# Optimization experiments

Hardware: AMD Instinct MI355X
Metric: run time of the kernel (lower is better)

The kernel has to match this reference:

```python
import jax, jax.numpy as jnp
import numpy as np
from jax import lax

WIRES = 4
EPS = 1e-5


def _conv2d(x, w, b):
    # x: [B,C,H,W], w: [O,I,3,3], SAME padding, stride 1
    y = lax.conv_general_dilated(x, w, (1, 1), 'SAME',
                                 dimension_numbers=('NCHW', 'OIHW', 'NCHW'))
    return y + b[None, :, None, None]


def _maxpool2(x):
    return lax.reduce_window(x, -jnp.inf, lax.max, (1, 1, 2, 2), (1, 1, 2, 2), 'VALID')


def _cnot_perm(c, t, n=WIRES):
    # wire 0 = most significant bit; CNOT is a self-inverse basis permutation
    idx = np.arange(2 ** n)
    cbit = (idx >> (n - 1 - c)) & 1
    flipped = idx ^ (1 << (n - 1 - t))
    return np.where(cbit == 1, flipped, idx)


_CNOT_PERMS = [_cnot_perm(c, c + 1) for c in range(WIRES - 1)]
_Z_SIGNS = np.stack([1.0 - 2.0 * ((np.arange(2 ** WIRES) >> (WIRES - 1 - i)) & 1)
                     for i in range(WIRES)], axis=1).astype(np.float32)  # [16, 4]


def _quantum_circuit(q_params, feats):
    # Batched state-vector sim of: RY(feats[i]) wire i; RX(params[i]) wire i;
    # CNOT chain; <Z_i>.  feats: [B,4], q_params: [4]
    hf = 0.5 * feats
    hp = 0.5 * q_params
    cy, sy = jnp.cos(hf), jnp.sin(hf)            # [B,4]
    cx, sx = jnp.cos(hp), jnp.sin(hp)            # [4]
    # per-wire state after RX @ RY |0>: amplitudes of |0>, |1>
    a0 = (cx * cy - 1j * sx * sy).astype(jnp.complex64)  # [B,4]
    a1 = (cx * sy - 1j * sx * cy).astype(jnp.complex64)  # [B,4]
    single = jnp.stack([a0, a1], axis=-1)        # [B,4,2]
    # product state -> full 16-dim state via successive outer products
    psi = single[:, 0]                           # [B,2]
    for i in range(1, WIRES):
        psi = (psi[:, :, None] * single[:, i][:, None, :]).reshape(psi.shape[0], -1)
    # CNOT chain = fixed basis permutations
    for perm in _CNOT_PERMS:
        psi = psi[:, perm]                       # [B,16]
    probs = psi.real ** 2 + psi.imag ** 2        # [B,16]
    return probs @ jnp.asarray(_Z_SIGNS)         # [B,4]


def setup_inputs() -> dict:
    key = jax.random.key(0)
    ks = jax.random.split(key, 8)
    B, C, H, W = 512, 1, 128, 128
    return {
        'x': jax.random.normal(ks[0], (B, C, H, W), jnp.float32),
        'conv1_w': jax.random.normal(ks[1], (8, C, 3, 3), jnp.float32) * 0.1,
        'conv1_b': jnp.zeros((8,), jnp.float32),
        'conv2_w': jax.random.normal(ks[2], (16, 8, 3, 3), jnp.float32) * 0.1,
        'conv2_b': jnp.zeros((16,), jnp.float32),
        'q_params': jax.random.normal(ks[3], (WIRES,), jnp.float32),
        'bn_gamma': jnp.ones((4,), jnp.float32),
        'bn_beta': jnp.zeros((4,), jnp.float32),
        'head_w': jax.random.normal(ks[4], (4, WIRES), jnp.float32) * 0.5,
        'head_b': jnp.zeros((4,), jnp.float32),
    }


def reference(x, conv1_w, conv1_b, conv2_w, conv2_b, q_params,
              bn_gamma, bn_beta, head_w, head_b):
    h = jax.nn.relu(_conv2d(x, conv1_w, conv1_b))
    h = _maxpool2(h)
    h = jax.nn.relu(_conv2d(h, conv2_w, conv2_b))
    h = _maxpool2(h)
    feats = h.mean(axis=(2, 3))                  # AdaptiveAvgPool2d(1) -> [B,16]
    q_out = _quantum_circuit(q_params, feats[:, :WIRES])  # [B,4]
    # BatchNorm1d (training mode, biased variance)
    mu = q_out.mean(axis=0)
    var = q_out.var(axis=0)
    normed = bn_gamma * (q_out - mu) / jnp.sqrt(var + EPS) + bn_beta
    return normed @ head_w.T + head_b
```

## Files before the change

### kernel.cpp

```cpp
#include <hip/hip_runtime.h>

#define EPS 1e-5f

typedef float f2 __attribute__((ext_vector_type(2)));
typedef float f4 __attribute__((ext_vector_type(4)));

__device__ __forceinline__ float uload(const float* __restrict__ p) {
  return __int_as_float(__builtin_amdgcn_readfirstlane(__float_as_int(*p)));
}

__global__ __launch_bounds__(256, 4) void k12_fused(
    const float* __restrict__ x, const float* __restrict__ w1,
    const float* __restrict__ b1, const float* __restrict__ w2,
    const float* __restrict__ b2, float* __restrict__ partials) {
  __shared__ float p1[8][18][66];
  __shared__ float wred[4][4];

  const int q   = blockIdx.x & 3;
  const int b   = blockIdx.x >> 2;
  const int tid = threadIdx.x;
  const float* xb = x + (size_t)b * (128 * 128);

  if (tid < 144) {
    int ic = tid / 18, gl = tid - ic * 18;
    p1[ic][gl][0]  = 0.f;
    p1[ic][gl][65] = 0.f;
  }

  float wv1[8][9], bb1[8];
#pragma unroll
  for (int oc = 0; oc < 8; ++oc) {
#pragma unroll
    for (int k = 0; k < 9; ++k) wv1[oc][k] = uload(w1 + oc * 9 + k);
    bb1[oc] = uload(b1 + oc);
  }

#pragma unroll 1
  for (int pos = tid; pos < 18 * 64; pos += 256) {
    const int gl = pos >> 6, px = pos & 63;
    const int G = 16 * q - 1 + gl;
    const bool validG = (G >= 0) && (G < 64);
    const int xr0 = 2 * G - 1;
    float xin[4][4];
#pragma unroll
    for (int r = 0; r < 4; ++r) {
      const int row = xr0 + r;
      const bool rok = validG && (row >= 0) && (row < 128);
      const float* rp = xb + row * 128;
#pragma unroll
      for (int c = 0; c < 4; ++c) {
        const int col = 2 * px - 1 + c;
        const bool ok = rok && (col >= 0) && (col < 128);
        xin[r][c] = ok ? rp[col] : 0.f;
      }
    }
#pragma unroll
    for (int oc = 0; oc < 8; ++oc) {
      float best = 0.f;
#pragma unroll
      for (int dy = 0; dy < 2; ++dy)
#pragma unroll
        for (int dx = 0; dx < 2; ++dx) {
          float a = bb1[oc];
#pragma unroll
          for (int ky = 0; ky < 3; ++ky)
#pragma unroll
            for (int kx = 0; kx < 3; ++kx)
              a = fmaf(xin[dy + ky][dx + kx], wv1[oc][ky * 3 + kx], a);
          best = fmaxf(best, a);
        }
      p1[oc][gl][px + 1] = validG ? best : 0.f;
    }
  }
  __syncthreads();

  const int px2  = tid & 31;
  const int py2l = tid >> 5;

  float acc[4][2][2];
#pragma unroll
  for (int oc = 0; oc < 4; ++oc) {
    float bias = uload(b2 + oc);
    acc[oc][0][0] = bias; acc[oc][0][1] = bias;
    acc[oc][1][0] = bias; acc[oc][1][1] = bias;
  }

#pragma unroll 1
  for (int ic = 0; ic < 8; ++ic) {
    float xin[4][4];
#pragma unroll
    for (int r = 0; r < 4; ++r) {
      const f2* rp = (const f2*)&p1[ic][2 * py2l + r][2 * px2];
      f2 v0 = rp[0], v1 = rp[1];
      xin[r][0] = v0.x; xin[r][1] = v0.y; xin[r][2] = v1.x; xin[r][3] = v1.y;
    }
#pragma unroll
    for (int oc = 0; oc < 4; ++oc) {
      float wv[9];
#pragma unroll
      for (int k = 0; k < 9; ++k) wv[k] = uload(w2 + (oc * 8 + ic) * 9 + k);
#pragma unroll
      for (int dy = 0; dy < 2; ++dy)
#pragma unroll
        for (int dx = 0; dx < 2; ++dx) {
#pragma unroll
          for (int ky = 0; ky < 3; ++ky)
#pragma unroll
            for (int kx = 0; kx < 3; ++kx)
              acc[oc][dy][dx] =
                  fmaf(xin[dy + ky][dx + kx], wv[ky * 3 + kx], acc[oc][dy][dx]);
        }
    }
  }

  const int lane = tid & 63, w = tid >> 6;
#pragma unroll
  for (int oc = 0; oc < 4; ++oc) {
    float p = fmaxf(fmaxf(fmaxf(acc[oc][0][0], acc[oc][0][1]),
                          fmaxf(acc[oc][1][0], acc[oc][1][1])), 0.f);
#pragma unroll
    for (int off = 32; off > 0; off >>= 1) p += __shfl_down(p, off);
    if (lane == 0) wred[w][oc] = p;
  }
  __syncthreads();
  if (tid < 4) {
    float s = wred[0][tid] + wred[1][tid] + wred[2][tid] + wred[3][tid];
    partials[((size_t)b * 4 + q) * 4 + tid] = s;
  }
}

__global__ __launch_bounds__(512) void k3_tail(
    const float* __restrict__ partials, const float* __restrict__ qp,
    const float* __restrict__ gamma, const float* __restrict__ beta,
    const float* __restrict__ hw, const float* __restrict__ hb,
    float* __restrict__ out) {
  __shared__ float wsum[8][8];
  __shared__ float stats[8];
  const int tid = threadIdx.x;

  const f4* pp = (const f4*)(partials + tid * 16);
  f4 s0 = pp[0], s1 = pp[1], s2 = pp[2], s3 = pp[3];
  float f[4];
  f[0] = (s0.x + s1.x + s2.x + s3.x) * (1.f / 1024.f);
  f[1] = (s0.y + s1.y + s2.y + s3.y) * (1.f / 1024.f);
  f[2] = (s0.z + s1.z + s2.z + s3.z) * (1.f / 1024.f);
  f[3] = (s0.w + s1.w + s2.w + s3.w) * (1.f / 1024.f);

  float a0r[4], a0i[4], a1r[4], a1i[4];
#pragma unroll
  for (int i = 0; i < 4; ++i) {
    float cy, sy, cx, sx;
    __sincosf(0.5f * f[i], &sy, &cy);
    __sincosf(0.5f * uload(qp + i), &sx, &cx);
    a0r[i] = cx * cy; a0i[i] = -sx * sy;
    a1r[i] = cx * sy; a1i[i] = -sx * cy;
  }

  float pr[16], pi[16];
#pragma unroll
  for (int j = 0; j < 16; ++j) {
    float rr = 1.f, ii = 0.f;
#pragma unroll
    for (int w = 0; w < 4; ++w) {
      int bit = (j >> (3 - w)) & 1;
      float ar = bit ? a1r[w] : a0r[w];
      float ai = bit ? a1i[w] : a0i[w];
      float t = rr * ar - ii * ai;
      ii = rr * ai + ii * ar;
      rr = t;
    }
    pr[j] = rr; pi[j] = ii;
  }

  constexpr int comp[16] = {0, 1, 3, 2, 6, 7, 5, 4, 12, 13, 15, 14, 10, 11, 9, 8};
  float qv[4] = {0.f, 0.f, 0.f, 0.f};
#pragma unroll
  for (int j = 0; j < 16; ++j) {
    int s = comp[j];
    float p = pr[s] * pr[s] + pi[s] * pi[s];
#pragma unroll
    for (int i = 0; i < 4; ++i)
      qv[i] += ((j >> (3 - i)) & 1) ? -p : p;
  }

  float v[8];
#pragma unroll
  for (int i = 0; i < 4; ++i) { v[i] = qv[i]; v[4 + i] = qv[i] * qv[i]; }
#pragma unroll
  for (int k = 0; k < 8; ++k)
#pragma unroll
    for (int off = 32; off > 0; off >>= 1) v[k] += __shfl_down(v[k], off);
  const int lane = tid & 63, w = tid >> 6;
  if (lane == 0) {
#pragma unroll
    for (int k = 0; k < 8; ++k) wsum[w][k] = v[k];
  }
  __syncthreads();
  if (tid < 8) {
    float s = 0.f;
#pragma unroll
    for (int ww = 0; ww < 8; ++ww) s += wsum[ww][tid];
    stats[tid] = s * (1.f / 512.f);
  }
  __syncthreads();

  float nm[4];
#pragma unroll
  for (int i = 0; i < 4; ++i) {
    float mu  = stats[i];
    float var = stats[4 + i] - mu * mu;
    nm[i] = uload(gamma + i) * (qv[i] - mu) * rsqrtf(var + EPS) + uload(beta + i);
  }
#pragma unroll
  for (int k = 0; k < 4; ++k) {
    float o = uload(hb + k);
#pragma unroll
    for (int i = 0; i < 4; ++i) o = fmaf(nm[i], uload(hw + k * 4 + i), o);
    out[tid * 4 + k] = o;
  }
}

extern "C" void kernel_launch(void* const* d_in, const int* in_sizes, int n_in,
                              void* d_out, int out_size, void* d_ws, size_t ws_size,
                              hipStream_t stream) {
  const float* x  = (const float*)d_in[0];
  const float* w1 = (const float*)d_in[1];
  const float* b1 = (const float*)d_in[2];
  const float* w2 = (const float*)d_in[3];
  const float* b2 = (const float*)d_in[4];
  const float* qp = (const float*)d_in[5];
  const float* gm = (const float*)d_in[6];
  const float* bt = (const float*)d_in[7];
  const float* hw = (const float*)d_in[8];
  const float* hb = (const float*)d_in[9];
  float* out = (float*)d_out;

  float* partials = (float*)d_ws;

  k12_fused<<<512 * 4, 256, 0, stream>>>(x, w1, b1, w2, b2, partials);
  k3_tail<<<1, 512, 0, stream>>>(partials, qp, gm, bt, hw, hb, out);
}
```

Before: 124.8 us.

## Stage input tile in LDS and split conv1/conv2 into two channel groups

Each block first copies its input row band (38x130 with zero halo) into shared memory, so conv1 reads LDS instead of gathering overlapping global loads. Conv1 and conv2 then run in two passes of four channels each, which halves the p1 buffer and keeps LDS use roughly the same. The conv2 weights and bias are staged into LDS rather than loaded as scalars each time. The cost is an extra barrier per group, more LDS traffic, and conv1 work split across two passes.

After: 138.5 us. 1.11x slower.

```diff
diff --git a/kernel.cpp b/kernel.cpp
--- a/kernel.cpp
+++ b/kernel.cpp
@@ -2,7 +2,6 @@
 
 #define EPS 1e-5f
 
-typedef float f2 __attribute__((ext_vector_type(2)));
 typedef float f4 __attribute__((ext_vector_type(4)));
 
 __device__ __forceinline__ float uload(const float* __restrict__ p) {
@@ -13,7 +12,9 @@
     const float* __restrict__ x, const float* __restrict__ w1,
     const float* __restrict__ b1, const float* __restrict__ w2,
     const float* __restrict__ b2, float* __restrict__ partials) {
-  __shared__ float p1[8][18][66];
+  __shared__ float xt[38][132];
+  __shared__ float p1[4][18][66];
+  __shared__ float w2s[292];
   __shared__ float wred[4][4];
 
   const int q   = blockIdx.x & 3;
@@ -21,95 +22,110 @@
   const int tid = threadIdx.x;
   const float* xb = x + (size_t)b * (128 * 128);
 
-  if (tid < 144) {
+  w2s[tid < 288 ? tid : 0] = w2[tid < 288 ? tid : 0];
+  if (tid < 32) w2s[256 + tid] = w2[256 + tid];
+  if (tid < 4)  w2s[288 + tid] = b2[tid];
+
+  if (tid < 72) {
     int ic = tid / 18, gl = tid - ic * 18;
     p1[ic][gl][0]  = 0.f;
     p1[ic][gl][65] = 0.f;
   }
 
-  float wv1[8][9], bb1[8];
-#pragma unroll
-  for (int oc = 0; oc < 8; ++oc) {
-#pragma unroll
-    for (int k = 0; k < 9; ++k) wv1[oc][k] = uload(w1 + oc * 9 + k);
-    bb1[oc] = uload(b1 + oc);
-  }
-
-#pragma unroll 1
-  for (int pos = tid; pos < 18 * 64; pos += 256) {
-    const int gl = pos >> 6, px = pos & 63;
-    const int G = 16 * q - 1 + gl;
-    const bool validG = (G >= 0) && (G < 64);
-    const int xr0 = 2 * G - 1;
-    float xin[4][4];
-#pragma unroll
-    for (int r = 0; r < 4; ++r) {
-      const int row = xr0 + r;
-      const bool rok = validG && (row >= 0) && (row < 128);
-      const float* rp = xb + row * 128;
-#pragma unroll
-      for (int c = 0; c < 4; ++c) {
-        const int col = 2 * px - 1 + c;
-        const bool ok = rok && (col >= 0) && (col < 128);
-        xin[r][c] = ok ? rp[col] : 0.f;
+  {
+    const int xr0 = 32 * q - 3;
+    int r = tid / 132, c = tid - r * 132;
+#pragma unroll
+    for (int it = 0; it < 20; ++it) {
+      if (r < 38) {
+        int gy = xr0 + r, gc = c - 1;
+        float v = 0.f;
+        if (gy >= 0 && gy < 128 && gc >= 0 && gc < 128) v = xb[gy * 128 + gc];
+        xt[r][c] = v;
       }
-    }
-#pragma unroll
-    for (int oc = 0; oc < 8; ++oc) {
-      float best = 0.f;
-#pragma unroll
-      for (int dy = 0; dy < 2; ++dy)
-#pragma unroll
-        for (int dx = 0; dx < 2; ++dx) {
-          float a = bb1[oc];
-#pragma unroll
-          for (int ky = 0; ky < 3; ++ky)
-#pragma unroll
-            for (int kx = 0; kx < 3; ++kx)
-              a = fmaf(xin[dy + ky][dx + kx], wv1[oc][ky * 3 + kx], a);
-          best = fmaxf(best, a);
-        }
-      p1[oc][gl][px + 1] = validG ? best : 0.f;
-    }
-  }
-  __syncthreads();
+      r += 1; c += 124;
+      if (c >= 132) { c -= 132; r += 1; }
+    }
+  }
+  __syncthreads();
+
+  float acc[4][2][2];
+#pragma unroll
+  for (int oc = 0; oc < 4; ++oc) {
+    float bias = w2s[288 + oc];
+    acc[oc][0][0] = bias; acc[oc][0][1] = bias;
+    acc[oc][1][0] = bias; acc[oc][1][1] = bias;
+  }
 
   const int px2  = tid & 31;
   const int py2l = tid >> 5;
 
-  float acc[4][2][2];
-#pragma unroll
-  for (int oc = 0; oc < 4; ++oc) {
-    float bias = uload(b2 + oc);
-    acc[oc][0][0] = bias; acc[oc][0][1] = bias;
-    acc[oc][1][0] = bias; acc[oc][1][1] = bias;
-  }
-
 #pragma unroll 1
-  for (int ic = 0; ic < 8; ++ic) {
-    float xin[4][4];
-#pragma unroll
-    for (int r = 0; r < 4; ++r) {
-      const f2* rp = (const f2*)&p1[ic][2 * py2l + r][2 * px2];
-      f2 v0 = rp[0], v1 = rp[1];
-      xin[r][0] = v0.x; xin[r][1] = v0.y; xin[r][2] = v1.x; xin[r][3] = v1.y;
-    }
+  for (int g = 0; g < 2; ++g) {
+    if (g) __syncthreads();
+
+    float wv1[4][9], bb1[4];
 #pragma unroll
     for (int oc = 0; oc < 4; ++oc) {
-      float wv[9];
-#pragma unroll
-      for (int k = 0; k < 9; ++k) wv[k] = uload(w2 + (oc * 8 + ic) * 9 + k);
-#pragma unroll
-      for (int dy = 0; dy < 2; ++dy)
-#pragma unroll
-        for (int dx = 0; dx < 2; ++dx) {
-#pragma unroll
-          for (int ky = 0; ky < 3; ++ky)
-#pragma unroll
-            for (int kx = 0; kx < 3; ++kx)
-              acc[oc][dy][dx] =
-                  fmaf(xin[dy + ky][dx + kx], wv[ky * 3 + kx], acc[oc][dy][dx]);
-        }
+#pragma unroll
+      for (int k = 0; k < 9; ++k) wv1[oc][k] = uload(w1 + (4 * g + oc) * 9 + k);
+      bb1[oc] = uload(b1 + 4 * g + oc);
+    }
+
+#pragma unroll 1
+    for (int pos = tid; pos < 18 * 64; pos += 256) {
+      const int gl = pos >> 6, px = pos & 63;
+      const int G = 16 * q - 1 + gl;
+      const bool validG = (G >= 0) && (G < 64);
+      float xin[4][4];
+#pragma unroll
+      for (int r = 0; r < 4; ++r)
+#pragma unroll
+        for (int c = 0; c < 4; ++c)
+          xin[r][c] = xt[2 * gl + r][2 * px + c];
+#pragma unroll
+      for (int oc = 0; oc < 4; ++oc) {
+        float best = 0.f;
+#pragma unroll
+        for (int dy = 0; dy < 2; ++dy)
+#pragma unroll
+          for (int dx = 0; dx < 2; ++dx) {
+            float a = bb1[oc];
+#pragma unroll
+            for (int ky = 0; ky < 3; ++ky)
+#pragma unroll
+              for (int kx = 0; kx < 3; ++kx)
+                a = fmaf(xin[dy + ky][dx + kx], wv1[oc][ky * 3 + kx], a);
+            best = fmaxf(best, a);
+          }
+        p1[oc][gl][px + 1] = validG ? best : 0.f;
+      }
+    }
+    __syncthreads();
+
+#pragma unroll 1
+    for (int ic = 0; ic < 4; ++ic) {
+      float xin[4][4];
+#pragma unroll
+      for (int r = 0; r < 4; ++r)
+#pragma unroll
+        for (int c = 0; c < 4; ++c)
+          xin[r][c] = p1[ic][2 * py2l + r][2 * px2 + c];
+#pragma unroll
+      for (int oc = 0; oc < 4; ++oc) {
+        const float* wp = &w2s[(oc * 8 + 4 * g + ic) * 9];
+#pragma unroll
+        for (int dy = 0; dy < 2; ++dy)
+#pragma unroll
+          for (int dx = 0; dx < 2; ++dx) {
+#pragma unroll
+            for (int ky = 0; ky < 3; ++ky)
+#pragma unroll
+              for (int kx = 0; kx < 3; ++kx)
+                acc[oc][dy][dx] =
+                    fmaf(xin[dy + ky][dx + kx], wp[ky * 3 + kx], acc[oc][dy][dx]);
+          }
+      }
     }
   }
 
```

## Split conv1 into two channel groups with halved LDS tile and smem weights

Applied to the files above, without the earlier changes.

Conv1 output channels are now computed in two passes of four channels, so the pooled conv1 tile in shared memory is half its former size. This allows six blocks per CU instead of four. Conv1 and conv2 weights and biases are staged once into padded shared arrays and read as vector loads, replacing scalar uniform global loads. Each conv1 thread now produces two adjacent pooled outputs from a float4-vectorized input row read. The cost is recomputing the input window loads twice, one per channel group, plus extra barriers.

Result: slower. 155.3 us (+24.4%).

```diff
diff --git a/kernel.cpp b/kernel.cpp
--- a/kernel.cpp
+++ b/kernel.cpp
@@ -9,11 +9,13 @@
   return __int_as_float(__builtin_amdgcn_readfirstlane(__float_as_int(*p)));
 }
 
-__global__ __launch_bounds__(256, 4) void k12_fused(
+__global__ __launch_bounds__(256, 6) void k12_fused(
     const float* __restrict__ x, const float* __restrict__ w1,
     const float* __restrict__ b1, const float* __restrict__ w2,
     const float* __restrict__ b2, float* __restrict__ partials) {
-  __shared__ float p1[8][18][66];
+  __shared__ float p1[4][18][66];
+  __shared__ float w1s[104];
+  __shared__ float w2s[392];
   __shared__ float wred[4][4];
 
   const int q   = blockIdx.x & 3;
@@ -21,56 +23,19 @@
   const int tid = threadIdx.x;
   const float* xb = x + (size_t)b * (128 * 128);
 
-  if (tid < 144) {
-    int ic = tid / 18, gl = tid - ic * 18;
-    p1[ic][gl][0]  = 0.f;
-    p1[ic][gl][65] = 0.f;
-  }
-
-  float wv1[8][9], bb1[8];
-#pragma unroll
-  for (int oc = 0; oc < 8; ++oc) {
-#pragma unroll
-    for (int k = 0; k < 9; ++k) wv1[oc][k] = uload(w1 + oc * 9 + k);
-    bb1[oc] = uload(b1 + oc);
-  }
-
-#pragma unroll 1
-  for (int pos = tid; pos < 18 * 64; pos += 256) {
-    const int gl = pos >> 6, px = pos & 63;
-    const int G = 16 * q - 1 + gl;
-    const bool validG = (G >= 0) && (G < 64);
-    const int xr0 = 2 * G - 1;
-    float xin[4][4];
-#pragma unroll
-    for (int r = 0; r < 4; ++r) {
-      const int row = xr0 + r;
-      const bool rok = validG && (row >= 0) && (row < 128);
-      const float* rp = xb + row * 128;
-#pragma unroll
-      for (int c = 0; c < 4; ++c) {
-        const int col = 2 * px - 1 + c;
-        const bool ok = rok && (col >= 0) && (col < 128);
-        xin[r][c] = ok ? rp[col] : 0.f;
-      }
-    }
-#pragma unroll
-    for (int oc = 0; oc < 8; ++oc) {
-      float best = 0.f;
-#pragma unroll
-      for (int dy = 0; dy < 2; ++dy)
-#pragma unroll
-        for (int dx = 0; dx < 2; ++dx) {
-          float a = bb1[oc];
-#pragma unroll
-          for (int ky = 0; ky < 3; ++ky)
-#pragma unroll
-            for (int kx = 0; kx < 3; ++kx)
-              a = fmaf(xin[dy + ky][dx + kx], wv1[oc][ky * 3 + kx], a);
-          best = fmaxf(best, a);
-        }
-      p1[oc][gl][px + 1] = validG ? best : 0.f;
-    }
+  if (tid < 72) w1s[(tid / 9) * 12 + tid % 9] = w1[tid];
+  if (tid >= 72 && tid < 80) w1s[(tid - 72) * 12 + 9] = b1[tid - 72];
+  {
+    int t = tid;
+    w2s[(t / 9) * 12 + t % 9] = w2[t];
+    t = tid + 256;
+    if (t < 288) w2s[(t / 9) * 12 + t % 9] = w2[t];
+  }
+  if (tid < 4) w2s[384 + tid] = b2[tid];
+  if (tid < 72) {
+    int ic = tid / 18, r = tid % 18;
+    p1[ic][r][0]  = 0.f;
+    p1[ic][r][65] = 0.f;
   }
   __syncthreads();
 
@@ -80,36 +45,94 @@
   float acc[4][2][2];
 #pragma unroll
   for (int oc = 0; oc < 4; ++oc) {
-    float bias = uload(b2 + oc);
+    float bias = w2s[384 + oc];
     acc[oc][0][0] = bias; acc[oc][0][1] = bias;
     acc[oc][1][0] = bias; acc[oc][1][1] = bias;
   }
 
 #pragma unroll 1
-  for (int ic = 0; ic < 8; ++ic) {
-    float xin[4][4];
-#pragma unroll
-    for (int r = 0; r < 4; ++r) {
-      const f2* rp = (const f2*)&p1[ic][2 * py2l + r][2 * px2];
-      f2 v0 = rp[0], v1 = rp[1];
-      xin[r][0] = v0.x; xin[r][1] = v0.y; xin[r][2] = v1.x; xin[r][3] = v1.y;
+  for (int g = 0; g < 2; ++g) {
+    if (g) __syncthreads();
+
+#pragma unroll 1
+    for (int pos = tid; pos < 576; pos += 256) {
+      const int gl = pos >> 5, i = pos & 31;
+      const int G  = 16 * q - 1 + gl;
+      const bool vG = ((unsigned)G) < 64u;
+      const int xr0 = 2 * G - 1;
+      float xin[4][6];
+#pragma unroll
+      for (int r = 0; r < 4; ++r) {
+        const int row  = xr0 + r;
+        const bool rok = vG && ((unsigned)row < 128u);
+        const int rowc = min(max(row, 0), 127);
+        const float* rp = xb + rowc * 128;
+        const float le = rp[(i == 0) ? 0 : (4 * i - 1)];
+        const f4 mid   = *(const f4*)(rp + 4 * i);
+        const float ri = rp[(i == 31) ? 127 : (4 * i + 4)];
+        xin[r][0] = (rok && i != 0)  ? le    : 0.f;
+        xin[r][1] = rok              ? mid.x : 0.f;
+        xin[r][2] = rok              ? mid.y : 0.f;
+        xin[r][3] = rok              ? mid.z : 0.f;
+        xin[r][4] = rok              ? mid.w : 0.f;
+        xin[r][5] = (rok && i != 31) ? ri    : 0.f;
+      }
+#pragma unroll
+      for (int oc = 0; oc < 4; ++oc) {
+        const int o = 4 * g + oc;
+        const f4 wA = *(const f4*)&w1s[o * 12];
+        const f4 wB = *(const f4*)&w1s[o * 12 + 4];
+        const f2 wC = *(const f2*)&w1s[o * 12 + 8];
+        const float wv[9] = {wA.x, wA.y, wA.z, wA.w, wB.x, wB.y, wB.z, wB.w, wC.x};
+#pragma unroll
+        for (int h = 0; h < 2; ++h) {
+          float best = 0.f;
+#pragma unroll
+          for (int dy = 0; dy < 2; ++dy)
+#pragma unroll
+            for (int dx = 0; dx < 2; ++dx) {
+              float a = wC.y;
+#pragma unroll
+              for (int ky = 0; ky < 3; ++ky)
+#pragma unroll
+                for (int kx = 0; kx < 3; ++kx)
+                  a = fmaf(xin[dy + ky][2 * h + dx + kx], wv[ky * 3 + kx], a);
+              best = fmaxf(best, a);
+            }
+          p1[oc][gl][2 * i + 1 + h] = vG ? best : 0.f;
+        }
+      }
     }
-#pragma unroll
-    for (int oc = 0; oc < 4; ++oc) {
-      float wv[9];
-#pragma unroll
-      for (int k = 0; k < 9; ++k) wv[k] = uload(w2 + (oc * 8 + ic) * 9 + k);
-#pragma unroll
-      for (int dy = 0; dy < 2; ++dy)
-#pragma unroll
-        for (int dx = 0; dx < 2; ++dx) {
-#pragma unroll
-          for (int ky = 0; ky < 3; ++ky)
-#pragma unroll
-            for (int kx = 0; kx < 3; ++kx)
-              acc[oc][dy][dx] =
-                  fmaf(xin[dy + ky][dx + kx], wv[ky * 3 + kx], acc[oc][dy][dx]);
-        }
+    __syncthreads();
+
+#pragma unroll 1
+    for (int ic = 0; ic < 4; ++ic) {
+      float xin[4][4];
+#pragma unroll
+      for (int r = 0; r < 4; ++r) {
+        const f2* rp = (const f2*)&p1[ic][2 * py2l + r][2 * px2];
+        f2 v0 = rp[0], v1 = rp[1];
+        xin[r][0] = v0.x; xin[r][1] = v0.y; xin[r][2] = v1.x; xin[r][3] = v1.y;
+      }
+#pragma unroll
+      for (int oc = 0; oc < 4; ++oc) {
+        const int wi = (oc * 8 + 4 * g + ic) * 12;
+        const f4 wA = *(const f4*)&w2s[wi];
+        const f4 wB = *(const f4*)&w2s[wi + 4];
+        const float w8 = w2s[wi + 8];
+        const float wv[9] = {wA.x, wA.y, wA.z, wA.w, wB.x, wB.y, wB.z, wB.w, w8};
+#pragma unroll
+        for (int dy = 0; dy < 2; ++dy)
+#pragma unroll
+          for (int dx = 0; dx < 2; ++dx) {
+#pragma unroll
+            for (int ky = 0; ky < 3; ++ky)
+#pragma unroll
+              for (int kx = 0; kx < 3; ++kx)
+                acc[oc][dy][dx] =
+                    fmaf(xin[dy + ky][dx + kx], wv[ky * 3 + kx], acc[oc][dy][dx]);
+          }
+      }
     }
   }
 
```
